# Kernel optimization log

Hardware: AMD Instinct MI355X
Metric: run time of the kernel (lower is better)

The kernel has to match this reference:

```python
import jax, jax.numpy as jnp
import numpy as np

N_NODES = 250000


def _gat_conv(x, src, dst, W, att_src, att_dst, bias, n_nodes):
    # PyG GATConv, heads=1, concat=True, negative_slope=0.2, self-loops already appended.
    h = x @ W                              # [N, 2]
    a_s = h @ att_src                      # [N]
    a_d = h @ att_dst                      # [N]
    e = jax.nn.leaky_relu(a_s[src] + a_d[dst], 0.2)   # [E]
    # segment softmax over incoming edges of each dst node
    m = jax.ops.segment_max(e, dst, num_segments=n_nodes)
    e = jnp.exp(e - m[dst])
    denom = jax.ops.segment_sum(e, dst, num_segments=n_nodes)
    alpha = e / (denom[dst] + 1e-16)       # [E]
    out = jax.ops.segment_sum(alpha[:, None] * h[src], dst, num_segments=n_nodes)
    return out + bias


def setup_inputs() -> dict:
    key = jax.random.key(0)
    ks = jax.random.split(key, 10)
    N, E = N_NODES, 16000000
    x = jax.random.normal(ks[0], (N, 4), dtype=jnp.float32)
    edge_index = jax.random.randint(ks[1], (2, E), 0, N, dtype=jnp.int64)
    def gat_params(k):
        k1, k2, k3 = jax.random.split(k, 3)
        return (jax.random.normal(k1, (2, 2), dtype=jnp.float32),
                jax.random.normal(k2, (2,), dtype=jnp.float32),
                jax.random.normal(k3, (2,), dtype=jnp.float32),
                jnp.zeros((2,), dtype=jnp.float32))
    W1, as1, ad1, b1 = gat_params(ks[2])
    W2, as2, ad2, b2 = gat_params(ks[3])
    return {"x": x, "edge_index": edge_index,
            "W_F1": W1, "att_src_F1": as1, "att_dst_F1": ad1, "bias_F1": b1,
            "W_F2": W2, "att_src_F2": as2, "att_dst_F2": ad2, "bias_F2": b2}


def reference(x, edge_index, W_F1, att_src_F1, att_dst_F1, bias_F1,
              W_F2, att_src_F2, att_dst_F2, bias_F2):
    n = x.shape[0]
    loop = jnp.arange(n, dtype=edge_index.dtype)
    src = jnp.concatenate([edge_index[0], loop])
    dst = jnp.concatenate([edge_index[1], loop])
    x1, x2 = x[:, :2], x[:, 2:]
    s_x = _gat_conv(x1, src, dst, W_F1, att_src_F1, att_dst_F1, bias_F1, n)
    t_x = _gat_conv(x1, src, dst, W_F2, att_src_F2, att_dst_F2, bias_F2, n)
    x1_new = x2 * jnp.exp(s_x) + t_x
    log_det = jnp.sum(s_x, axis=1)
    return (x1_new, x2, log_det)
```

## Files before the change

### kernel.cpp

```cpp
#include <hip/hip_runtime.h>


#define BSH 8
#define BSZ 256
#define NB  977
#define CAP 17408
#define EPB 16384
#define P1T 1024
#define P2T 1024
#define MPT 17

typedef int  iv4 __attribute__((ext_vector_type(4)));
typedef _Float16 h4 __attribute__((ext_vector_type(4)));

static __device__ __forceinline__ float lrelu(float z) { return z > 0.f ? z : 0.2f * z; }

__global__ void __launch_bounds__(256) prep_kernel(
    const float* __restrict__ x, int N,
    const float* __restrict__ W1, const float* __restrict__ as1, const float* __restrict__ ad1,
    const float* __restrict__ W2, const float* __restrict__ as2, const float* __restrict__ ad2,
    h4* __restrict__ nodeSh, float4* __restrict__ nodeD,
    unsigned* __restrict__ cursor, float* __restrict__ acc, int zero_acc)
{
    int i = blockIdx.x * blockDim.x + threadIdx.x;
    if (i < NB) cursor[i] = (unsigned)i * CAP;
    if (i >= N) return;
    float x0 = x[4 * i], x1v = x[4 * i + 1];
    float cs1_0 = W1[0] * as1[0] + W1[1] * as1[1];
    float cs1_1 = W1[2] * as1[0] + W1[3] * as1[1];
    float cd1_0 = W1[0] * ad1[0] + W1[1] * ad1[1];
    float cd1_1 = W1[2] * ad1[0] + W1[3] * ad1[1];
    float cs2_0 = W2[0] * as2[0] + W2[1] * as2[1];
    float cs2_1 = W2[2] * as2[0] + W2[3] * as2[1];
    float cd2_0 = W2[0] * ad2[0] + W2[1] * ad2[1];
    float cd2_1 = W2[2] * ad2[0] + W2[3] * ad2[1];
    nodeSh[i] = (h4){ (_Float16)x0, (_Float16)x1v,
                      (_Float16)(x0 * cs1_0 + x1v * cs1_1),
                      (_Float16)(x0 * cs2_0 + x1v * cs2_1) };
    nodeD[i] = make_float4(x0 * cd1_0 + x1v * cd1_1, x0 * cd2_0 + x1v * cd2_1,
                           x[4 * i + 2], x[4 * i + 3]);
    if (zero_acc) {
        acc[i] = 0.f; acc[N + i] = 0.f; acc[2 * N + i] = 0.f;
        acc[3 * N + i] = 0.f; acc[4 * N + i] = 0.f; acc[5 * N + i] = 0.f;
    }
}

__global__ void __launch_bounds__(P1T) bin_kernel(
    const int* __restrict__ ei, int E,
    unsigned* __restrict__ bins, unsigned* __restrict__ cursor)
{
    __shared__ unsigned sorted[EPB];
    __shared__ unsigned lhist[NB];
    __shared__ unsigned lbase[NB];
    __shared__ unsigned sbase[NB + 1];
    __shared__ unsigned swv[16];

    int tid = threadIdx.x;
    for (int i = tid; i < NB; i += P1T) { lhist[i] = 0u; lbase[i] = 0u; }
    __syncthreads();

    const iv4* s4 = (const iv4*)ei;
    const iv4* d4 = (const iv4*)(ei + E);
    long long vbase = ((long long)blockIdx.x * EPB) >> 2;

    iv4 dv[4];
    unsigned rkp[8];
#pragma unroll
    for (int j = 0; j < 4; ++j) {
        long long v = vbase + (long long)j * P1T + tid;
        if (v * 4 < (long long)E) dv[j] = __builtin_nontemporal_load(&d4[v]);
        else dv[j] = (iv4){-1, -1, -1, -1};
        int dd[4] = { dv[j].x, dv[j].y, dv[j].z, dv[j].w };
#pragma unroll
        for (int k = 0; k < 4; ++k) {
            unsigned r = 0;
            if (dd[k] >= 0) r = atomicAdd(&lhist[((unsigned)dd[k]) >> BSH], 1u);
            int idx = j * 4 + k;
            if (idx & 1) rkp[idx >> 1] |= (r << 16);
            else         rkp[idx >> 1] = r;
        }
    }
    __syncthreads();

    {
        unsigned v = (tid < NB) ? lhist[tid] : 0u;
        unsigned lane = (unsigned)tid & 63u;
        unsigned inc = v;
#pragma unroll
        for (int off = 1; off < 64; off <<= 1) {
            unsigned u = __shfl_up(inc, off, 64);
            if (lane >= (unsigned)off) inc += u;
        }
        if (lane == 63u) swv[tid >> 6] = inc;
        __syncthreads();
        if (tid == 0) {
            unsigned s = 0;
            sbase[0] = 0;
#pragma unroll
            for (int w = 0; w < 16; ++w) { unsigned t = swv[w]; swv[w] = s; s += t; }
        }
        __syncthreads();
        if (tid < NB) {
            sbase[tid + 1] = inc + swv[tid >> 6];
            unsigned c = lhist[tid];
            if (c) lbase[tid] = atomicAdd(&cursor[tid], c);
        }
    }
    __syncthreads();

#pragma unroll
    for (int j = 0; j < 4; ++j) {
        long long v = vbase + (long long)j * P1T + tid;
        iv4 sv = (iv4){0, 0, 0, 0};
        if (v * 4 < (long long)E) sv = __builtin_nontemporal_load(&s4[v]);
        int ss[4] = { sv.x, sv.y, sv.z, sv.w };
        int dd[4] = { dv[j].x, dv[j].y, dv[j].z, dv[j].w };
#pragma unroll
        for (int k = 0; k < 4; ++k) {
            if (dd[k] >= 0) {
                unsigned b = ((unsigned)dd[k]) >> BSH;
                int idx = j * 4 + k;
                unsigned r = (idx & 1) ? (rkp[idx >> 1] >> 16) : (rkp[idx >> 1] & 0xFFFFu);
                sorted[sbase[b] + r] = ((unsigned)ss[k] << BSH) | ((unsigned)dd[k] & (BSZ - 1u));
            }
        }
    }
    __syncthreads();

    int wid = tid >> 6;
    unsigned lane = (unsigned)tid & 63u;
    for (int b = wid; b < NB; b += 16) {
        unsigned L  = lhist[b];
        unsigned gb = lbase[b];
        unsigned sb = sbase[b];
        unsigned lim = ((unsigned)b + 1u) * CAP;
        for (unsigned off = lane; off < L; off += 64u) {
            unsigned p = gb + off;
            if (p < lim) bins[p] = sorted[sb + off];
        }
    }
}

__global__ void __launch_bounds__(P2T) reduce_kernel(
    const unsigned* __restrict__ bins, const unsigned* __restrict__ cursor,
    const h4* __restrict__ nodeSh, const float4* __restrict__ nodeD, int N,
    const float* __restrict__ W1, const float* __restrict__ b1,
    const float* __restrict__ W2, const float* __restrict__ b2,
    float* __restrict__ out)
{
    __shared__ unsigned sorted[CAP];
    __shared__ unsigned hist[BSZ];
    __shared__ unsigned sbase[BSZ + 1];
    __shared__ unsigned swv[BSZ / 64];
    __shared__ float4   sD[BSZ];

    int b = blockIdx.x, tid = threadIdx.x;
    int node0 = b << BSH;
    unsigned start = (unsigned)b * CAP;
    unsigned cnt = cursor[b] - start;
    if (cnt > CAP) cnt = CAP;

    if (tid < BSZ) {
        hist[tid] = 0u;
        int n = node0 + tid;
        sD[tid] = (n < N) ? nodeD[n] : make_float4(0.f, 0.f, 0.f, 0.f);
    }
    __syncthreads();

    unsigned ev[MPT];
    unsigned rkp[(MPT + 1) / 2];
#pragma unroll
    for (int j = 0; j < MPT; ++j) {
        unsigned i = (unsigned)tid + (unsigned)j * P2T;
        unsigned e = 0xFFFFFFFFu, r = 0;
        if (i < cnt) {
            e = __builtin_nontemporal_load(&bins[start + i]);
            r = atomicAdd(&hist[e & (BSZ - 1u)], 1u);
        }
        ev[j] = e;
        if (j & 1) rkp[j >> 1] |= (r << 16);
        else       rkp[j >> 1] = r;
    }
    __syncthreads();

    if (tid < BSZ) {
        unsigned v = hist[tid];
        unsigned lane = (unsigned)tid & 63u;
#pragma unroll
        for (int off = 1; off < 64; off <<= 1) {
            unsigned u = __shfl_up(v, off, 64);
            if (lane >= (unsigned)off) v += u;
        }
        if (lane == 63u) swv[tid >> 6] = v;
        sbase[tid + 1] = v;
    }
    __syncthreads();
    if (tid == 0) {
        unsigned s = 0;
        sbase[0] = 0;
#pragma unroll
        for (int w = 0; w < BSZ / 64; ++w) { unsigned t = swv[w]; swv[w] = s; s += t; }
    }
    __syncthreads();
    if (tid < BSZ) sbase[tid + 1] += swv[tid >> 6];
    __syncthreads();

#pragma unroll
    for (int j = 0; j < MPT; ++j) {
        if (ev[j] != 0xFFFFFFFFu) {
            unsigned r = (j & 1) ? (rkp[j >> 1] >> 16) : (rkp[j >> 1] & 0xFFFFu);
            sorted[sbase[ev[j] & (BSZ - 1u)] + r] = ev[j];
        }
    }
    __syncthreads();

    int ln = tid >> 2;
    int q  = tid & 3;
    int n = node0 + ln;
    float4 Dv = sD[ln];
    float a0 = 0.f, a1 = 0.f, a2 = 0.f, a3 = 0.f, a4 = 0.f, a5 = 0.f;
    if (n < N) {
        unsigned beg = sbase[ln], end = sbase[ln + 1];
        unsigned i = beg + (unsigned)q;
        for (; i + 12u < end; i += 16u) {
            unsigned e0 = sorted[i];
            unsigned e1 = sorted[i + 4u];
            unsigned e2 = sorted[i + 8u];
            unsigned e3 = sorted[i + 12u];
            h4 S0 = nodeSh[e0 >> BSH];
            h4 S1 = nodeSh[e1 >> BSH];
            h4 S2 = nodeSh[e2 >> BSH];
            h4 S3 = nodeSh[e3 >> BSH];
            float w;
            w = __expf(lrelu((float)S0.z + Dv.x)); a0 += w * (float)S0.x; a1 += w * (float)S0.y; a2 += w;
            w = __expf(lrelu((float)S0.w + Dv.y)); a3 += w * (float)S0.x; a4 += w * (float)S0.y; a5 += w;
            w = __expf(lrelu((float)S1.z + Dv.x)); a0 += w * (float)S1.x; a1 += w * (float)S1.y; a2 += w;
            w = __expf(lrelu((float)S1.w + Dv.y)); a3 += w * (float)S1.x; a4 += w * (float)S1.y; a5 += w;
            w = __expf(lrelu((float)S2.z + Dv.x)); a0 += w * (float)S2.x; a1 += w * (float)S2.y; a2 += w;
            w = __expf(lrelu((float)S2.w + Dv.y)); a3 += w * (float)S2.x; a4 += w * (float)S2.y; a5 += w;
            w = __expf(lrelu((float)S3.z + Dv.x)); a0 += w * (float)S3.x; a1 += w * (float)S3.y; a2 += w;
            w = __expf(lrelu((float)S3.w + Dv.y)); a3 += w * (float)S3.x; a4 += w * (float)S3.y; a5 += w;
        }
        for (; i < end; i += 4u) {
            unsigned e = sorted[i];
            h4 S = nodeSh[e >> BSH];
            float w1 = __expf(lrelu((float)S.z + Dv.x));
            float w2 = __expf(lrelu((float)S.w + Dv.y));
            float sx = (float)S.x, sy = (float)S.y;
            a0 += w1 * sx; a1 += w1 * sy; a2 += w1;
            a3 += w2 * sx; a4 += w2 * sy; a5 += w2;
        }
    }
    a0 += __shfl_xor(a0, 1); a0 += __shfl_xor(a0, 2);
    a1 += __shfl_xor(a1, 1); a1 += __shfl_xor(a1, 2);
    a2 += __shfl_xor(a2, 1); a2 += __shfl_xor(a2, 2);
    a3 += __shfl_xor(a3, 1); a3 += __shfl_xor(a3, 2);
    a4 += __shfl_xor(a4, 1); a4 += __shfl_xor(a4, 2);
    a5 += __shfl_xor(a5, 1); a5 += __shfl_xor(a5, 2);
    if (q == 0 && n < N) {
        h4 S = nodeSh[n];
        float w1s = __expf(lrelu((float)S.z + Dv.x));
        float w2s = __expf(lrelu((float)S.w + Dv.y));
        float n1x = a0 + w1s * (float)S.x;
        float n1y = a1 + w1s * (float)S.y;
        float d1  = a2 + w1s + 1e-16f;
        float n2x = a3 + w2s * (float)S.x;
        float n2y = a4 + w2s * (float)S.y;
        float d2  = a5 + w2s + 1e-16f;
        float inv1 = 1.0f / d1, inv2 = 1.0f / d2;
        float s0 = (n1x * W1[0] + n1y * W1[2]) * inv1 + b1[0];
        float s1 = (n1x * W1[1] + n1y * W1[3]) * inv1 + b1[1];
        float t0 = (n2x * W2[0] + n2y * W2[2]) * inv2 + b2[0];
        float t1 = (n2x * W2[1] + n2y * W2[3]) * inv2 + b2[1];
        float x2a = Dv.z, x2b = Dv.w;
        out[2 * n]             = x2a * __expf(s0) + t0;
        out[2 * n + 1]         = x2b * __expf(s1) + t1;
        out[2 * N + 2 * n]     = x2a;
        out[2 * N + 2 * n + 1] = x2b;
        out[4 * N + n]         = s0 + s1;
    }
}

__global__ void __launch_bounds__(256) edge_kernel(
    const int* __restrict__ ei, int E, int N,
    const h4* __restrict__ nodeSh, const float4* __restrict__ nodeD,
    float* __restrict__ acc)
{
    int e = blockIdx.x * blockDim.x + threadIdx.x;
    if (e >= E) return;
    int s = ei[e];
    int d = ei[E + e];
    h4 S = nodeSh[s];
    float4 D = nodeD[d];
    float w1 = __expf(lrelu((float)S.z + D.x));
    float w2 = __expf(lrelu((float)S.w + D.y));
    unsafeAtomicAdd(&acc[d],         w1 * (float)S.x);
    unsafeAtomicAdd(&acc[N + d],     w1 * (float)S.y);
    unsafeAtomicAdd(&acc[2 * N + d], w1);
    unsafeAtomicAdd(&acc[3 * N + d], w2 * (float)S.x);
    unsafeAtomicAdd(&acc[4 * N + d], w2 * (float)S.y);
    unsafeAtomicAdd(&acc[5 * N + d], w2);
}

__global__ void __launch_bounds__(256) fin_kernel(
    int N,
    const float* __restrict__ W1, const float* __restrict__ b1,
    const float* __restrict__ W2, const float* __restrict__ b2,
    const h4* __restrict__ nodeSh, const float4* __restrict__ nodeD,
    const float* __restrict__ acc, float* __restrict__ out)
{
    int i = blockIdx.x * blockDim.x + threadIdx.x;
    if (i >= N) return;
    h4 S = nodeSh[i];
    float4 D = nodeD[i];
    float w1s = __expf(lrelu((float)S.z + D.x));
    float w2s = __expf(lrelu((float)S.w + D.y));
    float n1x = acc[i] + w1s * (float)S.x;
    float n1y = acc[N + i] + w1s * (float)S.y;
    float d1  = acc[2 * N + i] + w1s + 1e-16f;
    float n2x = acc[3 * N + i] + w2s * (float)S.x;
    float n2y = acc[4 * N + i] + w2s * (float)S.y;
    float d2  = acc[5 * N + i] + w2s + 1e-16f;
    float inv1 = 1.0f / d1, inv2 = 1.0f / d2;
    float s0 = (n1x * W1[0] + n1y * W1[2]) * inv1 + b1[0];
    float s1 = (n1x * W1[1] + n1y * W1[3]) * inv1 + b1[1];
    float t0 = (n2x * W2[0] + n2y * W2[2]) * inv2 + b2[0];
    float t1 = (n2x * W2[1] + n2y * W2[3]) * inv2 + b2[1];
    float x2a = D.z, x2b = D.w;
    out[2 * i]             = x2a * __expf(s0) + t0;
    out[2 * i + 1]         = x2b * __expf(s1) + t1;
    out[2 * N + 2 * i]     = x2a;
    out[2 * N + 2 * i + 1] = x2b;
    out[4 * N + i]         = s0 + s1;
}

extern "C" void kernel_launch(void* const* d_in, const int* in_sizes, int n_in,
                              void* d_out, int out_size, void* d_ws, size_t ws_size,
                              hipStream_t stream)
{
    const float* x   = (const float*)d_in[0];
    const int*   ei  = (const int*)d_in[1];
    const float* W1  = (const float*)d_in[2];
    const float* as1 = (const float*)d_in[3];
    const float* ad1 = (const float*)d_in[4];
    const float* b1  = (const float*)d_in[5];
    const float* W2  = (const float*)d_in[6];
    const float* as2 = (const float*)d_in[7];
    const float* ad2 = (const float*)d_in[8];
    const float* b2  = (const float*)d_in[9];

    int N = in_sizes[0] / 4;
    int E = in_sizes[1] / 2;

    char* ws = (char*)d_ws;
    h4*       nodeSh = (h4*)ws;
    float4*   nodeD  = (float4*)(ws + (size_t)8 * N);
    size_t    off_c  = ((size_t)24 * N + 255) & ~(size_t)255;
    unsigned* cursor = (unsigned*)(ws + off_c);
    size_t    off_b  = (off_c + 4 * NB + 255) & ~(size_t)255;
    unsigned* bins   = (unsigned*)(ws + off_b);
    float*    acc    = (float*)(ws + off_b);
    float*    out    = (float*)d_out;

    size_t need = off_b + (size_t)4 * NB * CAP;
    int nb = (N + 255) / 256;

    if (ws_size >= need && (E % 4) == 0) {
        prep_kernel<<<nb, 256, 0, stream>>>(x, N, W1, as1, ad1, W2, as2, ad2,
                                            nodeSh, nodeD, cursor, nullptr, 0);
        int gb = (E + EPB - 1) / EPB;
        bin_kernel<<<gb, P1T, 0, stream>>>(ei, E, bins, cursor);
        reduce_kernel<<<NB, P2T, 0, stream>>>(bins, cursor, nodeSh, nodeD, N,
                                              W1, b1, W2, b2, out);
    } else {
        prep_kernel<<<nb, 256, 0, stream>>>(x, N, W1, as1, ad1, W2, as2, ad2,
                                            nodeSh, nodeD, cursor, acc, 1);
        int eb = (E + 255) / 256;
        edge_kernel<<<eb, 256, 0, stream>>>(ei, E, N, nodeSh, nodeD, acc);
        fin_kernel<<<nb, 256, 0, stream>>>(N, W1, b1, W2, b2, nodeSh, nodeD, acc, out);
    }
}
```

Measured before the change: 351.5 us.

## Fuse node prep into bin kernel, double edges per block, memset cursors

```diff
diff --git a/kernel.cpp b/kernel.cpp
--- a/kernel.cpp
+++ b/kernel.cpp
@@ -5,7 +5,7 @@
 #define BSZ 256
 #define NB  977
 #define CAP 17408
-#define EPB 16384
+#define EPB 32768
 #define P1T 1024
 #define P2T 1024
 #define MPT 17
@@ -15,38 +15,12 @@
 
 static __device__ __forceinline__ float lrelu(float z) { return z > 0.f ? z : 0.2f * z; }
 
-__global__ void __launch_bounds__(256) prep_kernel(
+__global__ void __launch_bounds__(P1T) bin_kernel(
+    const int* __restrict__ ei, int E,
     const float* __restrict__ x, int N,
     const float* __restrict__ W1, const float* __restrict__ as1, const float* __restrict__ ad1,
     const float* __restrict__ W2, const float* __restrict__ as2, const float* __restrict__ ad2,
     h4* __restrict__ nodeSh, float4* __restrict__ nodeD,
-    unsigned* __restrict__ cursor, float* __restrict__ acc, int zero_acc)
-{
-    int i = blockIdx.x * blockDim.x + threadIdx.x;
-    if (i < NB) cursor[i] = (unsigned)i * CAP;
-    if (i >= N) return;
-    float x0 = x[4 * i], x1v = x[4 * i + 1];
-    float cs1_0 = W1[0] * as1[0] + W1[1] * as1[1];
-    float cs1_1 = W1[2] * as1[0] + W1[3] * as1[1];
-    float cd1_0 = W1[0] * ad1[0] + W1[1] * ad1[1];
-    float cd1_1 = W1[2] * ad1[0] + W1[3] * ad1[1];
-    float cs2_0 = W2[0] * as2[0] + W2[1] * as2[1];
-    float cs2_1 = W2[2] * as2[0] + W2[3] * as2[1];
-    float cd2_0 = W2[0] * ad2[0] + W2[1] * ad2[1];
-    float cd2_1 = W2[2] * ad2[0] + W2[3] * ad2[1];
-    nodeSh[i] = (h4){ (_Float16)x0, (_Float16)x1v,
-                      (_Float16)(x0 * cs1_0 + x1v * cs1_1),
-                      (_Float16)(x0 * cs2_0 + x1v * cs2_1) };
-    nodeD[i] = make_float4(x0 * cd1_0 + x1v * cd1_1, x0 * cd2_0 + x1v * cd2_1,
-                           x[4 * i + 2], x[4 * i + 3]);
-    if (zero_acc) {
-        acc[i] = 0.f; acc[N + i] = 0.f; acc[2 * N + i] = 0.f;
-        acc[3 * N + i] = 0.f; acc[4 * N + i] = 0.f; acc[5 * N + i] = 0.f;
-    }
-}
-
-__global__ void __launch_bounds__(P1T) bin_kernel(
-    const int* __restrict__ ei, int E,
     unsigned* __restrict__ bins, unsigned* __restrict__ cursor)
 {
     __shared__ unsigned sorted[EPB];
@@ -56,20 +30,45 @@
     __shared__ unsigned swv[16];
 
     int tid = threadIdx.x;
-    for (int i = tid; i < NB; i += P1T) { lhist[i] = 0u; lbase[i] = 0u; }
+
+    {
+        int i = blockIdx.x * 512 + (tid & 511);
+        if (tid < 512 && i < N) {
+            float4 xv = ((const float4*)x)[i];
+            float x0 = xv.x, x1v = xv.y;
+            float cs1_0 = W1[0] * as1[0] + W1[1] * as1[1];
+            float cs1_1 = W1[2] * as1[0] + W1[3] * as1[1];
+            float cd1_0 = W1[0] * ad1[0] + W1[1] * ad1[1];
+            float cd1_1 = W1[2] * ad1[0] + W1[3] * ad1[1];
+            float cs2_0 = W2[0] * as2[0] + W2[1] * as2[1];
+            float cs2_1 = W2[2] * as2[0] + W2[3] * as2[1];
+            float cd2_0 = W2[0] * ad2[0] + W2[1] * ad2[1];
+            float cd2_1 = W2[2] * ad2[0] + W2[3] * ad2[1];
+            nodeSh[i] = (h4){ (_Float16)x0, (_Float16)x1v,
+                              (_Float16)(x0 * cs1_0 + x1v * cs1_1),
+                              (_Float16)(x0 * cs2_0 + x1v * cs2_1) };
+            nodeD[i] = make_float4(x0 * cd1_0 + x1v * cd1_1, x0 * cd2_0 + x1v * cd2_1,
+                                   xv.z, xv.w);
+        }
+    }
+
+    for (int i = tid; i < NB; i += P1T) lhist[i] = 0u;
     __syncthreads();
 
     const iv4* s4 = (const iv4*)ei;
     const iv4* d4 = (const iv4*)(ei + E);
     long long vbase = ((long long)blockIdx.x * EPB) >> 2;
 
-    iv4 dv[4];
-    unsigned rkp[8];
-#pragma unroll
-    for (int j = 0; j < 4; ++j) {
+    iv4 dv[8];
+#pragma unroll
+    for (int j = 0; j < 8; ++j) {
         long long v = vbase + (long long)j * P1T + tid;
         if (v * 4 < (long long)E) dv[j] = __builtin_nontemporal_load(&d4[v]);
         else dv[j] = (iv4){-1, -1, -1, -1};
+    }
+    unsigned rkp[16];
+#pragma unroll
+    for (int j = 0; j < 8; ++j) {
         int dd[4] = { dv[j].x, dv[j].y, dv[j].z, dv[j].w };
 #pragma unroll
         for (int k = 0; k < 4; ++k) {
@@ -103,17 +102,21 @@
         if (tid < NB) {
             sbase[tid + 1] = inc + swv[tid >> 6];
             unsigned c = lhist[tid];
-            if (c) lbase[tid] = atomicAdd(&cursor[tid], c);
-        }
-    }
-    __syncthreads();
-
-#pragma unroll
-    for (int j = 0; j < 4; ++j) {
+            if (c) lbase[tid] = (unsigned)tid * CAP + atomicAdd(&cursor[tid], c);
+        }
+    }
+    __syncthreads();
+
+    iv4 sv[8];
+#pragma unroll
+    for (int j = 0; j < 8; ++j) {
         long long v = vbase + (long long)j * P1T + tid;
-        iv4 sv = (iv4){0, 0, 0, 0};
-        if (v * 4 < (long long)E) sv = __builtin_nontemporal_load(&s4[v]);
-        int ss[4] = { sv.x, sv.y, sv.z, sv.w };
+        if (v * 4 < (long long)E) sv[j] = __builtin_nontemporal_load(&s4[v]);
+        else sv[j] = (iv4){0, 0, 0, 0};
+    }
+#pragma unroll
+    for (int j = 0; j < 8; ++j) {
+        int ss[4] = { sv[j].x, sv[j].y, sv[j].z, sv[j].w };
         int dd[4] = { dv[j].x, dv[j].y, dv[j].z, dv[j].w };
 #pragma unroll
         for (int k = 0; k < 4; ++k) {
@@ -133,11 +136,10 @@
         unsigned L  = lhist[b];
         unsigned gb = lbase[b];
         unsigned sb = sbase[b];
-        unsigned lim = ((unsigned)b + 1u) * CAP;
-        for (unsigned off = lane; off < L; off += 64u) {
-            unsigned p = gb + off;
-            if (p < lim) bins[p] = sorted[sb + off];
-        }
+        unsigned room = ((unsigned)b + 1u) * CAP - gb;
+        if (L > room) L = room;
+        for (unsigned off = lane; off < L; off += 64u)
+            bins[gb + off] = sorted[sb + off];
     }
 }
 
@@ -157,7 +159,7 @@
     int b = blockIdx.x, tid = threadIdx.x;
     int node0 = b << BSH;
     unsigned start = (unsigned)b * CAP;
-    unsigned cnt = cursor[b] - start;
+    unsigned cnt = cursor[b];
     if (cnt > CAP) cnt = CAP;
 
     if (tid < BSZ) {
@@ -168,16 +170,16 @@
     __syncthreads();
 
     unsigned ev[MPT];
-    unsigned rkp[(MPT + 1) / 2];
 #pragma unroll
     for (int j = 0; j < MPT; ++j) {
         unsigned i = (unsigned)tid + (unsigned)j * P2T;
-        unsigned e = 0xFFFFFFFFu, r = 0;
-        if (i < cnt) {
-            e = __builtin_nontemporal_load(&bins[start + i]);
-            r = atomicAdd(&hist[e & (BSZ - 1u)], 1u);
-        }
-        ev[j] = e;
+        ev[j] = (i < cnt) ? __builtin_nontemporal_load(&bins[start + i]) : 0xFFFFFFFFu;
+    }
+    unsigned rkp[(MPT + 1) / 2];
+#pragma unroll
+    for (int j = 0; j < MPT; ++j) {
+        unsigned r = 0;
+        if (ev[j] != 0xFFFFFFFFu) r = atomicAdd(&hist[ev[j] & (BSZ - 1u)], 1u);
         if (j & 1) rkp[j >> 1] |= (r << 16);
         else       rkp[j >> 1] = r;
     }
@@ -281,6 +283,32 @@
     }
 }
 
+__global__ void __launch_bounds__(256) prep_kernel(
+    const float* __restrict__ x, int N,
+    const float* __restrict__ W1, const float* __restrict__ as1, const float* __restrict__ ad1,
+    const float* __restrict__ W2, const float* __restrict__ as2, const float* __restrict__ ad2,
+    h4* __restrict__ nodeSh, float4* __restrict__ nodeD, float* __restrict__ acc)
+{
+    int i = blockIdx.x * blockDim.x + threadIdx.x;
+    if (i >= N) return;
+    float4 xv = ((const float4*)x)[i];
+    float x0 = xv.x, x1v = xv.y;
+    float cs1_0 = W1[0] * as1[0] + W1[1] * as1[1];
+    float cs1_1 = W1[2] * as1[0] + W1[3] * as1[1];
+    float cd1_0 = W1[0] * ad1[0] + W1[1] * ad1[1];
+    float cd1_1 = W1[2] * ad1[0] + W1[3] * ad1[1];
+    float cs2_0 = W2[0] * as2[0] + W2[1] * as2[1];
+    float cs2_1 = W2[2] * as2[0] + W2[3] * as2[1];
+    float cd2_0 = W2[0] * ad2[0] + W2[1] * ad2[1];
+    float cd2_1 = W2[2] * ad2[0] + W2[3] * ad2[1];
+    nodeSh[i] = (h4){ (_Float16)x0, (_Float16)x1v,
+                      (_Float16)(x0 * cs1_0 + x1v * cs1_1),
+                      (_Float16)(x0 * cs2_0 + x1v * cs2_1) };
+    nodeD[i] = make_float4(x0 * cd1_0 + x1v * cd1_1, x0 * cd2_0 + x1v * cd2_1, xv.z, xv.w);
+    acc[i] = 0.f; acc[N + i] = 0.f; acc[2 * N + i] = 0.f;
+    acc[3 * N + i] = 0.f; acc[4 * N + i] = 0.f; acc[5 * N + i] = 0.f;
+}
+
 __global__ void __launch_bounds__(256) edge_kernel(
     const int* __restrict__ ei, int E, int N,
     const h4* __restrict__ nodeSh, const float4* __restrict__ nodeD,
@@ -363,18 +391,18 @@
     float*    out    = (float*)d_out;
 
     size_t need = off_b + (size_t)4 * NB * CAP;
-    int nb = (N + 255) / 256;
-
-    if (ws_size >= need && (E % 4) == 0) {
-        prep_kernel<<<nb, 256, 0, stream>>>(x, N, W1, as1, ad1, W2, as2, ad2,
-                                            nodeSh, nodeD, cursor, nullptr, 0);
-        int gb = (E + EPB - 1) / EPB;
-        bin_kernel<<<gb, P1T, 0, stream>>>(ei, E, bins, cursor);
+    int gb = (E + EPB - 1) / EPB;
+
+    if (ws_size >= need && (E % 4) == 0 && (size_t)gb * 512 >= (size_t)N) {
+        hipMemsetAsync(cursor, 0, sizeof(unsigned) * NB, stream);
+        bin_kernel<<<gb, P1T, 0, stream>>>(ei, E, x, N, W1, as1, ad1, W2, as2, ad2,
+                                           nodeSh, nodeD, bins, cursor);
         reduce_kernel<<<NB, P2T, 0, stream>>>(bins, cursor, nodeSh, nodeD, N,
                                               W1, b1, W2, b2, out);
     } else {
+        int nb = (N + 255) / 256;
         prep_kernel<<<nb, 256, 0, stream>>>(x, N, W1, as1, ad1, W2, as2, ad2,
-                                            nodeSh, nodeD, cursor, acc, 1);
+                                            nodeSh, nodeD, acc);
         int eb = (E + 255) / 256;
         edge_kernel<<<eb, 256, 0, stream>>>(ei, E, N, nodeSh, nodeD, acc);
         fin_kernel<<<nb, 256, 0, stream>>>(N, W1, b1, W2, b2, nodeSh, nodeD, acc, out);
```

Result: faster. 316.2 us (-10.1%).
